# Optimization experiments

Hardware: AMD Instinct MI355X
Metric: run time of the kernel (lower is better)

Reference implementation:

```python
import jax, jax.numpy as jnp
import numpy as np

OUT, IN = 4096, 4096      # weight_shape
VDIM = 8                  # codebook vector_dim
CODEBOOK_SIZE = 256
LEVEL = 2                 # haar_decomposition_level
INV_SQRT2 = 0.7071067811865476


def unpack_bool(packed, shape):
    # packed: int array of bytes (values 0..255); unpack 8 bits per byte (LSB first)
    bits = (packed[:, None] >> jnp.arange(8, dtype=packed.dtype)) & 1  # [n_bytes, 8]
    return bits.reshape(shape)


def inverse_haar(c, level):
    # c: [..., n] orthonormal Haar coefficients laid out [a_L, d_L, d_{L-1}, ..., d_1]
    n = c.shape[-1]
    m = n >> level
    a = c[..., :m]
    while m < n:
        d = c[..., m:2 * m]
        even = (a + d) * INV_SQRT2
        odd = (a - d) * INV_SQRT2
        a = jnp.stack([even, odd], axis=-1).reshape(c.shape[:-1] + (2 * m,))
        m *= 2
    return a


def setup_inputs() -> dict:
    key = jax.random.key(0)
    k1, k2, k3, k4, k5 = jax.random.split(key, 5)
    x = jax.random.normal(k1, (4, 2048, IN), dtype=jnp.float32)
    codebook = jax.random.normal(k2, (CODEBOOK_SIZE, VDIM), dtype=jnp.float32)
    scales = jax.random.uniform(k5, (OUT, 1), dtype=jnp.float32)
    indices = jax.random.randint(k3, (OUT * IN // VDIM,), 0, CODEBOOK_SIZE, dtype=jnp.int32)
    signs_packed = jax.random.randint(k4, (OUT * IN // 8,), 0, 256, dtype=jnp.int32)
    return {"x": x, "codebook": codebook, "scales": scales,
            "indices": indices, "signs_packed": signs_packed}


def reference(x, codebook, scales, indices, signs_packed):
    # codebook gather -> haar-domain magnitudes, reshaped to signs_shape = weight shape
    haar_freq = codebook[indices].reshape(OUT, IN)
    # unpack sign bits and map {0,1} -> {-1,+1}
    signs = 2.0 * unpack_bool(signs_packed, (OUT, IN)).astype(haar_freq.dtype) - 1.0
    haar_freq = haar_freq * signs
    # multi-level inverse Haar wavelet along in_features
    w = inverse_haar(haar_freq, LEVEL)
    w = w * scales  # per-output-row scales
    return jnp.einsum('bsi,oi->bso', x, w)
```

## Files before the change

kernel.cpp:

```cpp
#include <hip/hip_runtime.h>
#include <hip/hip_bf16.h>

typedef unsigned short u16;
typedef unsigned int u32;
typedef float f32x4 __attribute__((ext_vector_type(4)));
typedef u16 u16x4 __attribute__((ext_vector_type(4)));
typedef u16 u16x8 __attribute__((ext_vector_type(8)));
typedef __bf16 bf16x8 __attribute__((ext_vector_type(8)));

#define OUT_DIM 4096
#define IN_DIM  4096
#define M_DIM   8192

__device__ __forceinline__ u16 f2bf(float f) {
  u32 u = __builtin_bit_cast(u32, f);
  return (u16)((u + 0x7FFFu + ((u >> 16) & 1u)) >> 16);
}

__global__ __launch_bounds__(256) void build_w_kernel(
    const float* __restrict__ codebook, const float* __restrict__ scales,
    const int* __restrict__ indices, const int* __restrict__ signs,
    u16* __restrict__ W) {
  __shared__ float c[IN_DIM];
  const int o   = blockIdx.x;
  const int tid = threadIdx.x;
  for (int g = tid; g < IN_DIM / 8; g += 256) {
    const int idx = indices[o * (IN_DIM / 8) + g];
    const int sp  = signs[o * (IN_DIM / 8) + g];
    f32x4 c0 = *(const f32x4*)&codebook[idx * 8];
    f32x4 c1 = *(const f32x4*)&codebook[idx * 8 + 4];
    float v[8] = {c0[0], c0[1], c0[2], c0[3], c1[0], c1[1], c1[2], c1[3]};
#pragma unroll
    for (int j = 0; j < 8; ++j)
      c[g * 8 + j] = ((sp >> j) & 1) ? v[j] : -v[j];
  }
  __syncthreads();
  const float scale = scales[o];
  const float S = 0.70710678118654752440f;
  for (int t = tid; t < IN_DIM / 4; t += 256) {
    float a   = c[t];
    float d1  = c[IN_DIM / 4 + t];
    float d2a = c[IN_DIM / 2 + 2 * t];
    float d2b = c[IN_DIM / 2 + 2 * t + 1];
    float e  = (a + d1) * S;
    float od = (a - d1) * S;
    u16x4 w;
    w[0] = f2bf((e  + d2a) * S * scale);
    w[1] = f2bf((e  - d2a) * S * scale);
    w[2] = f2bf((od + d2b) * S * scale);
    w[3] = f2bf((od - d2b) * S * scale);
    *(u16x4*)&W[(size_t)o * IN_DIM + 4 * t] = w;
  }
}

__global__ __launch_bounds__(256) void cvt_x_kernel(
    const float* __restrict__ X, u16* __restrict__ Xb) {
  const int stride = gridDim.x * blockDim.x;
  const int n8 = (M_DIM * IN_DIM) / 8;
  for (int i = blockIdx.x * blockDim.x + threadIdx.x; i < n8; i += stride) {
    f32x4 a = *(const f32x4*)&X[(size_t)i * 8];
    f32x4 b = *(const f32x4*)&X[(size_t)i * 8 + 4];
    u16x8 r;
    r[0] = f2bf(a[0]); r[1] = f2bf(a[1]); r[2] = f2bf(a[2]); r[3] = f2bf(a[3]);
    r[4] = f2bf(b[0]); r[5] = f2bf(b[1]); r[6] = f2bf(b[2]); r[7] = f2bf(b[3]);
    *(u16x8*)&Xb[(size_t)i * 8] = r;
  }
}

__global__ __launch_bounds__(512, 1) void gemm_bt_kernel(
    const u16* __restrict__ A,
    const u16* __restrict__ B,
    float*     __restrict__ C) {
  constexpr int K   = IN_DIM;
  constexpr int NT  = K / 64;
  constexpr int NIT = NT / 2;
  extern __shared__ char smem[];

  const int tid  = threadIdx.x;
  const int wave = tid >> 6;
  const int lane = tid & 63;

  const int swz = (blockIdx.x & 7) * 64 + (blockIdx.x >> 3);
  const int bm = (swz >> 4) * 256;
  const int bn = (swz & 15) * 256;

  const int wr  = (wave >> 2) * 128;
  const int wc  = (wave & 3) * 64;
  const int fr  = lane & 15;
  const int fkB = (lane >> 4) * 16;

  int offA[2][4], offB[4];
#pragma unroll
  for (int mq = 0; mq < 2; ++mq)
#pragma unroll
    for (int m = 0; m < 4; ++m) {
      int o = (wr + mq * 64 + m * 16 + fr) * 64 + fkB;
      offA[mq][m] = o ^ ((o >> 3) & 0x30);
    }
#pragma unroll
  for (int n = 0; n < 4; ++n) {
    int o = (wc + n * 16 + fr) * 64 + fkB;
    offB[n] = 16384 + (o ^ ((o >> 3) & 0x30));
  }

  const int d0 = tid * 16,        d1 = 8192 + tid * 16;
  const int l0 = d0 ^ ((d0 >> 3) & 0x30), l1 = d1 ^ ((d1 >> 3) & 0x30);
  const u16* srcA0 = A + (size_t)(bm + (d0 >> 6)) * K + ((l0 & 63) >> 1);
  const u16* srcA1 = A + (size_t)(bm + (d1 >> 6)) * K + ((l1 & 63) >> 1);
  const u16* srcB0 = B + (size_t)(bn + (d0 >> 6)) * K + ((l0 & 63) >> 1);
  const u16* srcB1 = B + (size_t)(bn + (d1 >> 6)) * K + ((l1 & 63) >> 1);
  const int ldsW = wave * 1024;

#define GLD(SRC, DST)                                              \
  __builtin_amdgcn_global_load_lds(                                \
      (const __attribute__((address_space(1))) void*)(SRC),        \
      (__attribute__((address_space(3))) void*)(DST), 16, 0, 0)

  auto stagePart = [&](int bufi, int ks, int part, int tile) {
    char* base = smem + bufi * 65536 + ks * 32768 + part * 16384 + ldsW;
    const u16* s0 = (part ? srcB0 : srcA0) + tile * 64 + ks * 32;
    const u16* s1 = (part ? srcB1 : srcA1) + tile * 64 + ks * 32;
    GLD(s0, base);
    GLD(s1, base + 8192);
  };

  f32x4 acc[8][4] = {};
  bf16x8 aq[4], bq[4];

  stagePart(0, 0, 0, 0); stagePart(0, 0, 1, 0);
  stagePart(0, 1, 0, 0); stagePart(0, 1, 1, 0);
  stagePart(1, 0, 0, 1); stagePart(1, 0, 1, 1);
  asm volatile("s_waitcnt vmcnt(4)" ::: "memory");
  __builtin_amdgcn_s_barrier();

#define PHASE(BUFI, KS, MQ, READB, STAGE, GATE)                              \
  {                                                                          \
    const char* rb = smem + (BUFI) * 65536 + (KS) * 32768;                   \
    if (READB) {                                                             \
      _Pragma("unroll")                                                      \
      for (int n = 0; n < 4; ++n) bq[n] = *(const bf16x8*)(rb + offB[n]);    \
    }                                                                        \
    _Pragma("unroll")                                                        \
    for (int m = 0; m < 4; ++m) aq[m] = *(const bf16x8*)(rb + offA[MQ][m]);  \
    STAGE;                                                                   \
    __builtin_amdgcn_s_barrier();                                            \
    asm volatile("s_waitcnt lgkmcnt(0)" ::: "memory");                       \
    __builtin_amdgcn_s_setprio(1);                                           \
    _Pragma("unroll")                                                        \
    for (int m = 0; m < 4; ++m)                                              \
      _Pragma("unroll")                                                      \
      for (int n = 0; n < 4; ++n)                                            \
        acc[(MQ) * 4 + m][n] = __builtin_amdgcn_mfma_f32_16x16x32_bf16(      \
            aq[m], bq[n], acc[(MQ) * 4 + m][n], 0, 0, 0);                    \
    __builtin_amdgcn_s_setprio(0);                                           \
    GATE;                                                                    \
    __builtin_amdgcn_s_barrier();                                            \
  }

  for (int i = 0; i < NIT; ++i) {
    const int t0 = 2 * i;
    const bool more = (i < NIT - 1);
    PHASE(0, 0, 0, 1, stagePart(1, 1, 0, t0 + 1), )
    PHASE(0, 0, 1, 0, stagePart(1, 1, 1, t0 + 1), )
    PHASE(0, 1, 0, 1, if (more) stagePart(0, 0, 0, t0 + 2), )
    PHASE(0, 1, 1, 0, if (more) stagePart(0, 0, 1, t0 + 2),
          if (more) { asm volatile("s_waitcnt vmcnt(4)" ::: "memory"); }
          else      { asm volatile("s_waitcnt vmcnt(0)" ::: "memory"); })
    PHASE(1, 0, 0, 1, if (more) stagePart(0, 1, 0, t0 + 2), )
    PHASE(1, 0, 1, 0, if (more) stagePart(0, 1, 1, t0 + 2), )
    PHASE(1, 1, 0, 1, if (more) stagePart(1, 0, 0, t0 + 3), )
    PHASE(1, 1, 1, 0, if (more) stagePart(1, 0, 1, t0 + 3),
          if (more) { asm volatile("s_waitcnt vmcnt(4)" ::: "memory"); }
          else      { asm volatile("s_waitcnt vmcnt(0)" ::: "memory"); })
  }
#undef PHASE
#undef GLD

#pragma unroll
  for (int h = 0; h < 8; ++h)
#pragma unroll
    for (int n = 0; n < 4; ++n) {
      const int col = bn + wc + n * 16 + fr;
#pragma unroll
      for (int j = 0; j < 4; ++j) {
        const int row = bm + wr + h * 16 + (lane >> 4) * 4 + j;
        C[(size_t)row * OUT_DIM + col] = acc[h][n][j];
      }
    }
}

extern "C" void kernel_launch(void* const* d_in, const int* in_sizes, int n_in,
                              void* d_out, int out_size, void* d_ws, size_t ws_size,
                              hipStream_t stream) {
  const float* x        = (const float*)d_in[0];
  const float* codebook = (const float*)d_in[1];
  const float* scales   = (const float*)d_in[2];
  const int*   indices  = (const int*)d_in[3];
  const int*   signs    = (const int*)d_in[4];
  float* out = (float*)d_out;

  u16* W  = (u16*)d_ws;
  u16* Xb = (u16*)d_ws + (size_t)OUT_DIM * IN_DIM;

  (void)hipFuncSetAttribute((const void*)gemm_bt_kernel,
                            hipFuncAttributeMaxDynamicSharedMemorySize, 131072);

  build_w_kernel<<<OUT_DIM, 256, 0, stream>>>(codebook, scales, indices, signs, W);
  cvt_x_kernel<<<2048, 256, 0, stream>>>(x, Xb);
  gemm_bt_kernel<<<(M_DIM / 256) * (OUT_DIM / 256), 512, 131072, stream>>>(Xb, W, out);
}
```

Before: 286.0 us.

## Double-buffer LDS fragment registers to overlap reads with MFMA in GEMM

The GEMM main loop now reads the next phase's A/B fragments from LDS into alternate register sets while the current phase's MFMAs run, using partial lgkmcnt waits and sched_barriers to pin the ordering. The last iteration is peeled so the loop needs no 'more' predicate, and the vmcnt gates move ahead of the barrier. This is meant to hide LDS read latency behind matrix math. It costs extra VGPRs for the second fragment set and relies on hand-counted waitcnt values, which risks races if the counts are wrong.

```diff
diff --git a/kernel.cpp b/kernel.cpp
--- a/kernel.cpp
+++ b/kernel.cpp
@@ -125,56 +125,78 @@
   };
 
   f32x4 acc[8][4] = {};
-  bf16x8 aq[4], bq[4];
+  bf16x8 aq0[4], aq1[4], bq0[4], bq1[4];
+
+#define GVM4 asm volatile("s_waitcnt vmcnt(4)" ::: "memory")
+#define GVM0 asm volatile("s_waitcnt vmcnt(0)" ::: "memory")
+#define GNOP
+
+#define PH(CA, CB, CMQ, RA, RB, RDB, TB, TK, TM, STAGE, GATE, LG)            \
+  {                                                                          \
+    const char* nrb = smem + (TB) * 65536 + (TK) * 32768;                    \
+    _Pragma("unroll")                                                        \
+    for (int m = 0; m < 4; ++m)                                              \
+      RA[m] = *(const bf16x8*)(nrb + offA[TM][m]);                           \
+    if (RDB) {                                                               \
+      _Pragma("unroll")                                                      \
+      for (int n = 0; n < 4; ++n)                                            \
+        RB[n] = *(const bf16x8*)(nrb + offB[n]);                             \
+    }                                                                        \
+    STAGE;                                                                   \
+    __builtin_amdgcn_sched_barrier(0);                                       \
+    GATE;                                                                    \
+    __builtin_amdgcn_s_barrier();                                            \
+    asm volatile("s_waitcnt lgkmcnt(" #LG ")" ::: "memory");                 \
+    __builtin_amdgcn_sched_barrier(0);                                       \
+    __builtin_amdgcn_s_setprio(1);                                           \
+    _Pragma("unroll")                                                        \
+    for (int m = 0; m < 4; ++m)                                              \
+      _Pragma("unroll")                                                      \
+      for (int n = 0; n < 4; ++n)                                            \
+        acc[(CMQ) * 4 + m][n] = __builtin_amdgcn_mfma_f32_16x16x32_bf16(     \
+            CA[m], CB[n], acc[(CMQ) * 4 + m][n], 0, 0, 0);                   \
+    __builtin_amdgcn_s_setprio(0);                                           \
+    __builtin_amdgcn_s_barrier();                                            \
+  }
 
   stagePart(0, 0, 0, 0); stagePart(0, 0, 1, 0);
   stagePart(0, 1, 0, 0); stagePart(0, 1, 1, 0);
   stagePart(1, 0, 0, 1); stagePart(1, 0, 1, 1);
   asm volatile("s_waitcnt vmcnt(4)" ::: "memory");
   __builtin_amdgcn_s_barrier();
-
-#define PHASE(BUFI, KS, MQ, READB, STAGE, GATE)                              \
-  {                                                                          \
-    const char* rb = smem + (BUFI) * 65536 + (KS) * 32768;                   \
-    if (READB) {                                                             \
-      _Pragma("unroll")                                                      \
-      for (int n = 0; n < 4; ++n) bq[n] = *(const bf16x8*)(rb + offB[n]);    \
-    }                                                                        \
-    _Pragma("unroll")                                                        \
-    for (int m = 0; m < 4; ++m) aq[m] = *(const bf16x8*)(rb + offA[MQ][m]);  \
-    STAGE;                                                                   \
-    __builtin_amdgcn_s_barrier();                                            \
-    asm volatile("s_waitcnt lgkmcnt(0)" ::: "memory");                       \
-    __builtin_amdgcn_s_setprio(1);                                           \
-    _Pragma("unroll")                                                        \
-    for (int m = 0; m < 4; ++m)                                              \
-      _Pragma("unroll")                                                      \
-      for (int n = 0; n < 4; ++n)                                            \
-        acc[(MQ) * 4 + m][n] = __builtin_amdgcn_mfma_f32_16x16x32_bf16(      \
-            aq[m], bq[n], acc[(MQ) * 4 + m][n], 0, 0, 0);                    \
-    __builtin_amdgcn_s_setprio(0);                                           \
-    GATE;                                                                    \
-    __builtin_amdgcn_s_barrier();                                            \
-  }
-
-  for (int i = 0; i < NIT; ++i) {
+#pragma unroll
+  for (int m = 0; m < 4; ++m) aq1[m] = *(const bf16x8*)(smem + offA[0][m]);
+#pragma unroll
+  for (int n = 0; n < 4; ++n) bq0[n] = *(const bf16x8*)(smem + offB[n]);
+
+  for (int i = 0; i < NIT - 1; ++i) {
     const int t0 = 2 * i;
-    const bool more = (i < NIT - 1);
-    PHASE(0, 0, 0, 1, stagePart(1, 1, 0, t0 + 1), )
-    PHASE(0, 0, 1, 0, stagePart(1, 1, 1, t0 + 1), )
-    PHASE(0, 1, 0, 1, if (more) stagePart(0, 0, 0, t0 + 2), )
-    PHASE(0, 1, 1, 0, if (more) stagePart(0, 0, 1, t0 + 2),
-          if (more) { asm volatile("s_waitcnt vmcnt(4)" ::: "memory"); }
-          else      { asm volatile("s_waitcnt vmcnt(0)" ::: "memory"); })
-    PHASE(1, 0, 0, 1, if (more) stagePart(0, 1, 0, t0 + 2), )
-    PHASE(1, 0, 1, 0, if (more) stagePart(0, 1, 1, t0 + 2), )
-    PHASE(1, 1, 0, 1, if (more) stagePart(1, 0, 0, t0 + 3), )
-    PHASE(1, 1, 1, 0, if (more) stagePart(1, 0, 1, t0 + 3),
-          if (more) { asm volatile("s_waitcnt vmcnt(4)" ::: "memory"); }
-          else      { asm volatile("s_waitcnt vmcnt(0)" ::: "memory"); })
-  }
-#undef PHASE
+    PH(aq1, bq0, 0, aq0, bq1, 0, 0, 0, 1, stagePart(1, 1, 0, t0 + 1), GVM4, 4)
+    PH(aq0, bq0, 1, aq1, bq1, 1, 0, 1, 0, stagePart(1, 1, 1, t0 + 1), GNOP, 8)
+    PH(aq1, bq1, 0, aq0, bq0, 0, 0, 1, 1, stagePart(0, 0, 0, t0 + 2), GVM4, 4)
+    PH(aq0, bq1, 1, aq1, bq0, 1, 1, 0, 0, stagePart(0, 0, 1, t0 + 2), GNOP, 8)
+    PH(aq1, bq0, 0, aq0, bq1, 0, 1, 0, 1, stagePart(0, 1, 0, t0 + 2), GVM4, 4)
+    PH(aq0, bq0, 1, aq1, bq1, 1, 1, 1, 0, stagePart(0, 1, 1, t0 + 2), GNOP, 8)
+    PH(aq1, bq1, 0, aq0, bq0, 0, 1, 1, 1, stagePart(1, 0, 0, t0 + 3), GVM4, 4)
+    PH(aq0, bq1, 1, aq1, bq0, 1, 0, 0, 0, stagePart(1, 0, 1, t0 + 3), GNOP, 8)
+  }
+
+  {
+    const int t0 = NT - 2;
+    PH(aq1, bq0, 0, aq0, bq1, 0, 0, 0, 1, stagePart(1, 1, 0, t0 + 1), GVM4, 4)
+    PH(aq0, bq0, 1, aq1, bq1, 1, 0, 1, 0, stagePart(1, 1, 1, t0 + 1), GNOP, 8)
+    PH(aq1, bq1, 0, aq0, bq0, 0, 0, 1, 1, GNOP, GVM4, 4)
+    PH(aq0, bq1, 1, aq1, bq0, 1, 1, 0, 0, GNOP, GNOP, 8)
+    PH(aq1, bq0, 0, aq0, bq1, 0, 1, 0, 1, GNOP, GVM0, 4)
+    PH(aq0, bq0, 1, aq1, bq1, 1, 1, 1, 0, GNOP, GNOP, 8)
+    PH(aq1, bq1, 0, aq0, bq0, 0, 1, 1, 1, GNOP, GNOP, 4)
+    PH(aq0, bq1, 1, aq1, bq0, 1, 0, 0, 0, GNOP, GNOP, 8)
+  }
+#undef PH
 #undef GLD
+#undef GVM4
+#undef GVM0
+#undef GNOP
 
 #pragma unroll
   for (int h = 0; h < 8; ++h)
```

Result: slower. 315.9 us (+10.5%).
